# Optimization experiments

Measured on AMD Instinct MI355X. Metric: run time of the kernel, lower is better.

The kernel has to match this reference:

```python
import jax, jax.numpy as jnp
import numpy as np

BS = 64          # BSR block size
B, D_IN, H, D_OUT = 4096, 1024, 4096, 1024
DENSITY = 0.5    # fraction of nonzero 64x64 blocks in fc2


def setup_inputs() -> dict:
    key = jax.random.key(0)
    ks = jax.random.split(key, 4)
    x = jax.random.normal(ks[0], (B, D_IN), jnp.float32)
    w1 = jax.random.normal(ks[1], (H, D_IN), jnp.float32) * (1.0 / np.sqrt(D_IN))
    b1 = jnp.zeros((H,), jnp.float32)
    w3 = jax.random.normal(ks[2], (D_OUT, H), jnp.float32) * (1.0 / np.sqrt(H))
    b3 = jnp.zeros((D_OUT,), jnp.float32)
    # Build BSR structure for fc2 weight [H, H]: block grid is (H//BS, H//BS)
    nbr, nbc = H // BS, H // BS
    rng = np.random.default_rng(0)
    mask = rng.random((nbr, nbc)) < DENSITY
    mask[:, 0] = True  # ensure each block row has at least one block
    crow = np.concatenate([[0], np.cumsum(mask.sum(axis=1))]).astype(np.int32)
    col = np.concatenate([np.nonzero(mask[r])[0] for r in range(nbr)]).astype(np.int32)
    nnzb = int(col.shape[0])
    values = jax.random.normal(ks[3], (nnzb, BS, BS), jnp.float32) * (1.0 / np.sqrt(H))
    return {
        "x": x, "w1": w1, "b1": b1,
        "values": values, "w3": w3, "b3": b3,
        "crow_indices": jnp.asarray(crow),
        "col_indices": jnp.asarray(col),
    }


def bsr_linear(x, crow, col, values, n_block_rows):
    """y = x @ W.T where W [out, in] is BSR with blocks values[nnzb, bs, bs]."""
    bsz = x.shape[0]
    bs = values.shape[1]
    nnzb = col.shape[0]
    # block row index of each nonzero block, from CSR row pointers
    block_row = jnp.searchsorted(crow, jnp.arange(nnzb, dtype=crow.dtype), side='right') - 1
    xb = x.reshape(bsz, -1, bs)            # [B, n_block_cols, bs]
    gath = xb[:, col]                      # [B, nnzb, bs] irregular gather
    # per-block contribution: block is W[row_blk, col_blk] of shape [bs_out, bs_in]
    contrib = jnp.einsum('bni,noi->nbo', gath, values)  # [nnzb, B, bs]
    yb = jax.ops.segment_sum(contrib, block_row, num_segments=n_block_rows)  # [nbr, B, bs]
    return yb.transpose(1, 0, 2).reshape(bsz, n_block_rows * bs)


def reference(x, w1, b1, values, w3, b3, crow_indices, col_indices):
    # Flatten is a no-op for 2D input
    h = jax.nn.relu(x @ w1.T + b1)                                   # fc1 + ReLU
    h = jax.nn.relu(bsr_linear(h, crow_indices, col_indices, values, H // BS))  # BSR fc2 + ReLU
    return h @ w3.T + b3                                             # fc3
```

## Files before the change

### kernel.cpp

```cpp
#include <hip/hip_runtime.h>
#include <hip/hip_bf16.h>
#include <stdint.h>


typedef __attribute__((ext_vector_type(4))) float f32x4;
typedef __attribute__((ext_vector_type(8))) __bf16 bf16x8;

#define DEV static __device__ __forceinline__

DEV ushort f2bf(float f) {
  union { float f; uint32_t u; } v; v.f = f;
  uint32_t r = v.u + 0x7fffu + ((v.u >> 16) & 1u);
  return (ushort)(r >> 16);
}

DEV void gld_lds16(const void* g, void* l) {
  __builtin_amdgcn_global_load_lds(
      (const __attribute__((address_space(1))) void*)g,
      (__attribute__((address_space(3))) void*)l, 16, 0, 0);
}

__global__ void cvt4_kernel(const float* __restrict__ s0, ushort* __restrict__ d0, int n0,
                            const float* __restrict__ s1, ushort* __restrict__ d1, int n1,
                            const float* __restrict__ s2, ushort* __restrict__ d2, int n2,
                            const float* __restrict__ s3, ushort* __restrict__ d3, int n3) {
  const int total = (n0 + n1 + n2 + n3) >> 2;
  for (int idx = blockIdx.x * blockDim.x + threadIdx.x; idx < total;
       idx += gridDim.x * blockDim.x) {
    int i = idx * 4;
    const float* s; ushort* d;
    if (i < n0)               { s = s0; d = d0; }
    else if ((i -= n0) < n1)  { s = s1; d = d1; }
    else if ((i -= n1) < n2)  { s = s2; d = d2; }
    else                      { i -= n2; s = s3; d = d3; }
    float4 v = *(const float4*)(s + i);
    ushort4 o;
    o.x = f2bf(v.x); o.y = f2bf(v.y); o.z = f2bf(v.z); o.w = f2bf(v.w);
    *(ushort4*)(d + i) = o;
  }
}

template <bool RELU, bool OUT_BF16>
__global__ __launch_bounds__(256)
void gemm_nt(const ushort* __restrict__ A, const ushort* __restrict__ W,
             const float* __restrict__ bias, void* __restrict__ Cv,
             int K, int lda, int ldw, int ldc) {
  __shared__ ushort As[128 * 64];
  __shared__ ushort Ws[128 * 64];
  const int tid = threadIdx.x;
  const int wid = tid >> 6, lane = tid & 63;
  const int wm = wid >> 1, wn = wid & 1;
  const int i0 = blockIdx.y * 128, j0 = blockIdx.x * 128;
  f32x4 acc[4][4] = {};

  const int lrow = lane >> 3;
  const int lcol = (lane & 7) * 16;

  for (int k0 = 0; k0 < K; k0 += 64) {
#pragma unroll
    for (int i = 0; i < 4; ++i) {
      int ch = wid * 4 + i;
      int row = ch * 8 + lrow;
      const char* ga = (const char*)A + ((size_t)(i0 + row) * lda + k0) * 2 + lcol;
      gld_lds16(ga, (char*)As + ch * 1024);
      const char* gw = (const char*)W + ((size_t)(j0 + row) * ldw + k0) * 2 + lcol;
      gld_lds16(gw, (char*)Ws + ch * 1024);
    }
    __syncthreads();
#pragma unroll
    for (int kk = 0; kk < 64; kk += 32) {
      const int cl = lane & 15;
      const int kg = kk + (lane >> 4) * 8;
      bf16x8 a[4], b[4];
#pragma unroll
      for (int m = 0; m < 4; ++m)
        a[m] = *(const bf16x8*)&As[(wm * 64 + m * 16 + cl) * 64 + kg];
#pragma unroll
      for (int n = 0; n < 4; ++n)
        b[n] = *(const bf16x8*)&Ws[(wn * 64 + n * 16 + cl) * 64 + kg];
#pragma unroll
      for (int m = 0; m < 4; ++m)
#pragma unroll
        for (int n = 0; n < 4; ++n)
          acc[m][n] = __builtin_amdgcn_mfma_f32_16x16x32_bf16(a[m], b[n], acc[m][n], 0, 0, 0);
    }
    __syncthreads();
  }

  const int cl = lane & 15, r4 = (lane >> 4) * 4;
#pragma unroll
  for (int n = 0; n < 4; ++n) {
    int col = j0 + wn * 64 + n * 16 + cl;
    float bv = bias ? bias[col] : 0.0f;
#pragma unroll
    for (int m = 0; m < 4; ++m) {
      int rowb = i0 + wm * 64 + m * 16 + r4;
#pragma unroll
      for (int r = 0; r < 4; ++r) {
        float v = acc[m][n][r] + bv;
        if (RELU) v = fmaxf(v, 0.0f);
        if (OUT_BF16)
          ((ushort*)Cv)[(size_t)(rowb + r) * ldc + col] = f2bf(v);
        else
          ((float*)Cv)[(size_t)(rowb + r) * ldc + col] = v;
      }
    }
  }
}

__global__ __launch_bounds__(256)
void bsr_gemm(const ushort* __restrict__ A, const ushort* __restrict__ V,
              const int* __restrict__ crow, const int* __restrict__ colind,
              ushort* __restrict__ C, int Hdim) {
  __shared__ ushort As[2][256 * 64];
  __shared__ ushort Vs[2][64 * 64];
  const int tid = threadIdx.x;
  const int wid = tid >> 6, lane = tid & 63;

  const int bid = blockIdx.x;
  const int xcd = bid & 7;
  const int j = bid >> 3;
  const int tile = xcd + 8 * (j & 1);
  const int br = j >> 1;
  const int i0 = tile * 256;

  f32x4 acc[4][4] = {};
  const int n0 = crow[br], n1 = crow[br + 1];

  const int lr = lane >> 3;
  const int gsw = ((lane & 7) ^ lr) * 16;

  auto stage = [&](int buf, int n) {
    const int c = colind[n];
    const char* Abase = (const char*)A + ((size_t)i0 * Hdim + (size_t)c * 64) * 2;
#pragma unroll
    for (int i = 0; i < 8; ++i) {
      int ch = wid * 8 + i;
      int row = ch * 8 + lr;
      gld_lds16(Abase + (size_t)row * Hdim * 2 + gsw, (char*)As[buf] + ch * 1024);
    }
    const char* Vbase = (const char*)V + (size_t)n * 8192;
#pragma unroll
    for (int i = 0; i < 2; ++i) {
      int ch = wid * 2 + i;
      int row = ch * 8 + lr;
      gld_lds16(Vbase + row * 128 + gsw, (char*)Vs[buf] + ch * 1024);
    }
  };

  auto compute = [&](int buf) {
#pragma unroll
    for (int kk = 0; kk < 64; kk += 32) {
      const int cl = lane & 15;
      const int kg = kk + (lane >> 4) * 8;
      const int kx = kg ^ ((cl & 7) << 3);
      bf16x8 a[4], b[4];
#pragma unroll
      for (int m = 0; m < 4; ++m) {
        int row = wid * 64 + m * 16 + cl;
        a[m] = *(const bf16x8*)&As[buf][row * 64 + kx];
      }
#pragma unroll
      for (int nn = 0; nn < 4; ++nn) {
        int row = nn * 16 + cl;
        b[nn] = *(const bf16x8*)&Vs[buf][row * 64 + kx];
      }
      __builtin_amdgcn_s_setprio(1);
#pragma unroll
      for (int m = 0; m < 4; ++m)
#pragma unroll
        for (int nn = 0; nn < 4; ++nn)
          acc[m][nn] = __builtin_amdgcn_mfma_f32_16x16x32_bf16(a[m], b[nn], acc[m][nn], 0, 0, 0);
      __builtin_amdgcn_s_setprio(0);
    }
  };

  int cur = 0;
  stage(0, n0);
  __syncthreads();
  for (int n = n0; n < n1; ++n) {
    if (n + 1 < n1) stage(cur ^ 1, n + 1);
    compute(cur);
    __syncthreads();
    cur ^= 1;
  }

  const int cl = lane & 15, r4 = (lane >> 4) * 4;
#pragma unroll
  for (int nn = 0; nn < 4; ++nn) {
    int col = br * 64 + nn * 16 + cl;
#pragma unroll
    for (int m = 0; m < 4; ++m) {
      int rowb = i0 + wid * 64 + m * 16 + r4;
#pragma unroll
      for (int r = 0; r < 4; ++r) {
        float v = fmaxf(acc[m][nn][r], 0.0f);
        C[(size_t)(rowb + r) * Hdim + col] = f2bf(v);
      }
    }
  }
}

extern "C" void kernel_launch(void* const* d_in, const int* in_sizes, int n_in,
                              void* d_out, int out_size, void* d_ws, size_t ws_size,
                              hipStream_t stream) {
  const float* x    = (const float*)d_in[0];
  const float* w1   = (const float*)d_in[1];
  const float* b1   = (const float*)d_in[2];
  const float* vals = (const float*)d_in[3];
  const float* w3   = (const float*)d_in[4];
  const float* b3   = (const float*)d_in[5];
  const int* crow   = (const int*)d_in[6];
  const int* colind = (const int*)d_in[7];

  const int Bb = 4096, Din = 1024, H = 4096, Dout = 1024;
  const int nnzb = in_sizes[7];

  char* ws = (char*)d_ws;
  ushort* xb  = (ushort*)ws; ws += (size_t)Bb * Din * 2;
  ushort* w1b = (ushort*)ws; ws += (size_t)H * Din * 2;
  ushort* w3b = (ushort*)ws; ws += (size_t)Dout * H * 2;
  ushort* vb  = (ushort*)ws; ws += (size_t)nnzb * 64 * 64 * 2;
  ushort* h1b = (ushort*)ws; ws += (size_t)Bb * H * 2;
  ushort* h2b = (ushort*)ws; ws += (size_t)Bb * H * 2;

  hipLaunchKernelGGL(cvt4_kernel, dim3(2048), dim3(256), 0, stream,
                     x,    xb,  Bb * Din,
                     w1,   w1b, H * Din,
                     w3,   w3b, Dout * H,
                     vals, vb,  nnzb * 4096);

  hipLaunchKernelGGL((gemm_nt<true, true>), dim3(H / 128, Bb / 128), dim3(256), 0, stream,
                     xb, w1b, b1, (void*)h1b, Din, Din, Din, H);
  hipLaunchKernelGGL(bsr_gemm, dim3((Bb / 256) * (H / 64)), dim3(256), 0, stream,
                     h1b, vb, crow, colind, h2b, H);
  hipLaunchKernelGGL((gemm_nt<false, false>), dim3(Dout / 128, Bb / 128), dim3(256), 0, stream,
                     h2b, w3b, b3, d_out, H, H, H, Dout);
}
```

Measured before the change: 247.4 us.

## Split-K the fc3 GEMM and halve the BSR GEMM row tile

fc3 (K=4096, only 256 tiles) is split into two K halves, each writing fp32 partials, and a combine kernel then adds the halves and the bias. This doubles the block count to fill the GPU, at the cost of extra fp32 partial writes and reads plus one more launch. The BSR GEMM tile shrinks from 256 to 128 rows, doubling grid size and cutting LDS use, and A and V staging is merged into one loop. Split-K runs only when the workspace is large enough.

```diff
diff --git a/kernel.cpp b/kernel.cpp
--- a/kernel.cpp
+++ b/kernel.cpp
@@ -40,6 +40,18 @@
   }
 }
 
+__global__ void combine_kernel(const float* __restrict__ p0, const float* __restrict__ p1,
+                               const float* __restrict__ bias, float* __restrict__ out,
+                               int total, int ncols) {
+  int i = (blockIdx.x * blockDim.x + threadIdx.x) * 4;
+  if (i >= total) return;
+  float4 a = *(const float4*)(p0 + i);
+  float4 b = *(const float4*)(p1 + i);
+  const float4 bv = *(const float4*)(bias + (i & (ncols - 1)));
+  a.x += b.x + bv.x; a.y += b.y + bv.y; a.z += b.z + bv.z; a.w += b.w + bv.w;
+  *(float4*)(out + i) = a;
+}
+
 template <bool RELU, bool OUT_BF16>
 __global__ __launch_bounds__(256)
 void gemm_nt(const ushort* __restrict__ A, const ushort* __restrict__ W,
@@ -109,10 +121,76 @@
 }
 
 __global__ __launch_bounds__(256)
+void gemm_nt_sk(const ushort* __restrict__ A, const ushort* __restrict__ W,
+                float* __restrict__ P0, float* __restrict__ P1,
+                int Khalf, int lda, int ldw, int ldc, int ntx) {
+  const int kidx = blockIdx.x / ntx;
+  const int bx = blockIdx.x % ntx;
+  const ushort* Ao = A + (size_t)kidx * Khalf;
+  const ushort* Wo = W + (size_t)kidx * Khalf;
+  float* P = kidx ? P1 : P0;
+
+  __shared__ ushort As[128 * 64];
+  __shared__ ushort Ws[128 * 64];
+  const int tid = threadIdx.x;
+  const int wid = tid >> 6, lane = tid & 63;
+  const int wm = wid >> 1, wn = wid & 1;
+  const int i0 = blockIdx.y * 128, j0 = bx * 128;
+  f32x4 acc[4][4] = {};
+
+  const int lrow = lane >> 3;
+  const int lcol = (lane & 7) * 16;
+
+  for (int k0 = 0; k0 < Khalf; k0 += 64) {
+#pragma unroll
+    for (int i = 0; i < 4; ++i) {
+      int ch = wid * 4 + i;
+      int row = ch * 8 + lrow;
+      const char* ga = (const char*)Ao + ((size_t)(i0 + row) * lda + k0) * 2 + lcol;
+      gld_lds16(ga, (char*)As + ch * 1024);
+      const char* gw = (const char*)Wo + ((size_t)(j0 + row) * ldw + k0) * 2 + lcol;
+      gld_lds16(gw, (char*)Ws + ch * 1024);
+    }
+    __syncthreads();
+#pragma unroll
+    for (int kk = 0; kk < 64; kk += 32) {
+      const int cl = lane & 15;
+      const int kg = kk + (lane >> 4) * 8;
+      bf16x8 a[4], b[4];
+#pragma unroll
+      for (int m = 0; m < 4; ++m)
+        a[m] = *(const bf16x8*)&As[(wm * 64 + m * 16 + cl) * 64 + kg];
+#pragma unroll
+      for (int n = 0; n < 4; ++n)
+        b[n] = *(const bf16x8*)&Ws[(wn * 64 + n * 16 + cl) * 64 + kg];
+#pragma unroll
+      for (int m = 0; m < 4; ++m)
+#pragma unroll
+        for (int n = 0; n < 4; ++n)
+          acc[m][n] = __builtin_amdgcn_mfma_f32_16x16x32_bf16(a[m], b[n], acc[m][n], 0, 0, 0);
+    }
+    __syncthreads();
+  }
+
+  const int cl = lane & 15, r4 = (lane >> 4) * 4;
+#pragma unroll
+  for (int n = 0; n < 4; ++n) {
+    int col = j0 + wn * 64 + n * 16 + cl;
+#pragma unroll
+    for (int m = 0; m < 4; ++m) {
+      int rowb = i0 + wm * 64 + m * 16 + r4;
+#pragma unroll
+      for (int r = 0; r < 4; ++r)
+        P[(size_t)(rowb + r) * ldc + col] = acc[m][n][r];
+    }
+  }
+}
+
+__global__ __launch_bounds__(256)
 void bsr_gemm(const ushort* __restrict__ A, const ushort* __restrict__ V,
               const int* __restrict__ crow, const int* __restrict__ colind,
               ushort* __restrict__ C, int Hdim) {
-  __shared__ ushort As[2][256 * 64];
+  __shared__ ushort As[2][128 * 64];
   __shared__ ushort Vs[2][64 * 64];
   const int tid = threadIdx.x;
   const int wid = tid >> 6, lane = tid & 63;
@@ -120,11 +198,11 @@
   const int bid = blockIdx.x;
   const int xcd = bid & 7;
   const int j = bid >> 3;
-  const int tile = xcd + 8 * (j & 1);
-  const int br = j >> 1;
-  const int i0 = tile * 256;
-
-  f32x4 acc[4][4] = {};
+  const int tile = xcd + 8 * (j & 3);
+  const int br = j >> 2;
+  const int i0 = tile * 128;
+
+  f32x4 acc[2][4] = {};
   const int n0 = crow[br], n1 = crow[br + 1];
 
   const int lr = lane >> 3;
@@ -133,18 +211,17 @@
   auto stage = [&](int buf, int n) {
     const int c = colind[n];
     const char* Abase = (const char*)A + ((size_t)i0 * Hdim + (size_t)c * 64) * 2;
-#pragma unroll
-    for (int i = 0; i < 8; ++i) {
-      int ch = wid * 8 + i;
-      int row = ch * 8 + lr;
-      gld_lds16(Abase + (size_t)row * Hdim * 2 + gsw, (char*)As[buf] + ch * 1024);
-    }
     const char* Vbase = (const char*)V + (size_t)n * 8192;
 #pragma unroll
-    for (int i = 0; i < 2; ++i) {
-      int ch = wid * 2 + i;
-      int row = ch * 8 + lr;
-      gld_lds16(Vbase + row * 128 + gsw, (char*)Vs[buf] + ch * 1024);
+    for (int i = 0; i < 6; ++i) {
+      int ch = wid * 6 + i;
+      if (ch < 16) {
+        int row = ch * 8 + lr;
+        gld_lds16(Abase + (size_t)row * Hdim * 2 + gsw, (char*)As[buf] + ch * 1024);
+      } else {
+        int vch = ch - 16;
+        gld_lds16(Vbase + (vch * 8 + lr) * 128 + gsw, (char*)Vs[buf] + vch * 1024);
+      }
     }
   };
 
@@ -154,20 +231,16 @@
       const int cl = lane & 15;
       const int kg = kk + (lane >> 4) * 8;
       const int kx = kg ^ ((cl & 7) << 3);
-      bf16x8 a[4], b[4];
-#pragma unroll
-      for (int m = 0; m < 4; ++m) {
-        int row = wid * 64 + m * 16 + cl;
-        a[m] = *(const bf16x8*)&As[buf][row * 64 + kx];
-      }
-#pragma unroll
-      for (int nn = 0; nn < 4; ++nn) {
-        int row = nn * 16 + cl;
-        b[nn] = *(const bf16x8*)&Vs[buf][row * 64 + kx];
-      }
+      bf16x8 a[2], b[4];
+#pragma unroll
+      for (int m = 0; m < 2; ++m)
+        a[m] = *(const bf16x8*)&As[buf][(wid * 32 + m * 16 + cl) * 64 + kx];
+#pragma unroll
+      for (int nn = 0; nn < 4; ++nn)
+        b[nn] = *(const bf16x8*)&Vs[buf][(nn * 16 + cl) * 64 + kx];
       __builtin_amdgcn_s_setprio(1);
 #pragma unroll
-      for (int m = 0; m < 4; ++m)
+      for (int m = 0; m < 2; ++m)
 #pragma unroll
         for (int nn = 0; nn < 4; ++nn)
           acc[m][nn] = __builtin_amdgcn_mfma_f32_16x16x32_bf16(a[m], b[nn], acc[m][nn], 0, 0, 0);
@@ -190,8 +263,8 @@
   for (int nn = 0; nn < 4; ++nn) {
     int col = br * 64 + nn * 16 + cl;
 #pragma unroll
-    for (int m = 0; m < 4; ++m) {
-      int rowb = i0 + wid * 64 + m * 16 + r4;
+    for (int m = 0; m < 2; ++m) {
+      int rowb = i0 + wid * 32 + m * 16 + r4;
 #pragma unroll
       for (int r = 0; r < 4; ++r) {
         float v = fmaxf(acc[m][nn][r], 0.0f);
@@ -217,12 +290,16 @@
   const int nnzb = in_sizes[7];
 
   char* ws = (char*)d_ws;
-  ushort* xb  = (ushort*)ws; ws += (size_t)Bb * Din * 2;
-  ushort* w1b = (ushort*)ws; ws += (size_t)H * Din * 2;
-  ushort* w3b = (ushort*)ws; ws += (size_t)Dout * H * 2;
-  ushort* vb  = (ushort*)ws; ws += (size_t)nnzb * 64 * 64 * 2;
-  ushort* h1b = (ushort*)ws; ws += (size_t)Bb * H * 2;
-  ushort* h2b = (ushort*)ws; ws += (size_t)Bb * H * 2;
+  size_t off = 0;
+  ushort* xb  = (ushort*)(ws + off); off += (size_t)Bb * Din * 2;
+  ushort* w1b = (ushort*)(ws + off); off += (size_t)H * Din * 2;
+  ushort* w3b = (ushort*)(ws + off); off += (size_t)Dout * H * 2;
+  ushort* vb  = (ushort*)(ws + off); off += (size_t)nnzb * 64 * 64 * 2;
+  ushort* h1b = (ushort*)(ws + off); off += (size_t)Bb * H * 2;
+  ushort* h2b = (ushort*)(ws + off); off += (size_t)Bb * H * 2;
+  float* p0 = (float*)(ws + off); off += (size_t)Bb * Dout * 4;
+  float* p1 = (float*)(ws + off); off += (size_t)Bb * Dout * 4;
+  const bool can_splitk = (off <= ws_size);
 
   hipLaunchKernelGGL(cvt4_kernel, dim3(2048), dim3(256), 0, stream,
                      x,    xb,  Bb * Din,
@@ -232,8 +309,16 @@
 
   hipLaunchKernelGGL((gemm_nt<true, true>), dim3(H / 128, Bb / 128), dim3(256), 0, stream,
                      xb, w1b, b1, (void*)h1b, Din, Din, Din, H);
-  hipLaunchKernelGGL(bsr_gemm, dim3((Bb / 256) * (H / 64)), dim3(256), 0, stream,
+  hipLaunchKernelGGL(bsr_gemm, dim3((Bb / 128) * (H / 64)), dim3(256), 0, stream,
                      h1b, vb, crow, colind, h2b, H);
-  hipLaunchKernelGGL((gemm_nt<false, false>), dim3(Dout / 128, Bb / 128), dim3(256), 0, stream,
-                     h2b, w3b, b3, d_out, H, H, H, Dout);
-}
+  if (can_splitk) {
+    hipLaunchKernelGGL(gemm_nt_sk, dim3(2 * (Dout / 128), Bb / 128), dim3(256), 0, stream,
+                       h2b, w3b, p0, p1, H / 2, H, H, Dout, Dout / 128);
+    int total = Bb * Dout;
+    hipLaunchKernelGGL(combine_kernel, dim3((total / 4 + 255) / 256), dim3(256), 0, stream,
+                       p0, p1, b3, (float*)d_out, total, Dout);
+  } else {
+    hipLaunchKernelGGL((gemm_nt<false, false>), dim3(Dout / 128, Bb / 128), dim3(256), 0, stream,
+                       h2b, w3b, b3, d_out, H, H, H, Dout);
+  }
+}
```

Result: faster. 234.9 us (-5.0%).
